# Kernel optimization log

Measured on AMD Instinct MI355X. Metric: run time of the kernel, lower is better.

Reference implementation:

```python
import jax, jax.numpy as jnp
import numpy as np

DIM = 256
NH = 8
HD = DIM // NH          # 32
KD = HD // 2            # 16, attn_ratio=0.5
SCALE = KD ** -0.5
EPS = 1e-3              # BatchNorm2d eps=0.001
B, H, W = 8, 32, 32


def _bn(x, g, b, m, v):
    # inference-mode BatchNorm2d over channel axis 1 of NCHW
    inv = g / jnp.sqrt(v + EPS)
    return x * inv[None, :, None, None] + (b - m * inv)[None, :, None, None]


def setup_inputs() -> dict:
    key = jax.random.key(0)
    ks = jax.random.split(key, 16)
    h_out = DIM + 2 * NH * KD  # 512
    return {
        "x": jax.random.normal(ks[0], (B, DIM, H, W), jnp.float32),
        "qkv_w": jax.random.normal(ks[1], (h_out, DIM), jnp.float32) * 0.05,
        "qkv_g": jax.random.uniform(ks[2], (h_out,), jnp.float32, 0.5, 1.5),
        "qkv_b": jax.random.normal(ks[3], (h_out,), jnp.float32) * 0.1,
        "qkv_m": jax.random.normal(ks[4], (h_out,), jnp.float32) * 0.1,
        "qkv_v": jax.random.uniform(ks[5], (h_out,), jnp.float32, 0.5, 1.5),
        "pe_w": jax.random.normal(ks[6], (DIM, 1, 3, 3), jnp.float32) * 0.1,
        "pe_g": jax.random.uniform(ks[7], (DIM,), jnp.float32, 0.5, 1.5),
        "pe_b": jax.random.normal(ks[8], (DIM,), jnp.float32) * 0.1,
        "pe_m": jax.random.normal(ks[9], (DIM,), jnp.float32) * 0.1,
        "pe_v": jax.random.uniform(ks[10], (DIM,), jnp.float32, 0.5, 1.5),
        "proj_w": jax.random.normal(ks[11], (DIM, DIM), jnp.float32) * 0.05,
        "proj_g": jax.random.uniform(ks[12], (DIM,), jnp.float32, 0.5, 1.5),
        "proj_b": jax.random.normal(ks[13], (DIM,), jnp.float32) * 0.1,
        "proj_m": jax.random.normal(ks[14], (DIM,), jnp.float32) * 0.1,
        "proj_v": jax.random.uniform(ks[15], (DIM,), jnp.float32, 0.5, 1.5),
    }


def reference(x, qkv_w, qkv_g, qkv_b, qkv_m, qkv_v,
              pe_w, pe_g, pe_b, pe_m, pe_v,
              proj_w, proj_g, proj_b, proj_m, proj_v):
    b, c, h, w = x.shape
    n = h * w
    # qkv: 1x1 conv (no bias) + BN, act=Identity
    qkv = _bn(jnp.einsum('oc,bchw->bohw', qkv_w, x), qkv_g, qkv_b, qkv_m, qkv_v)
    qkv = qkv.reshape(b, NH, 2 * KD + HD, n)
    q, k, v = jnp.split(qkv, [KD, 2 * KD], axis=2)  # [b,nh,kd,n],[b,nh,kd,n],[b,nh,hd,n]
    # attn = q^T @ k * scale, softmax over keys (last dim)
    attn = jax.nn.softmax(jnp.einsum('bhkn,bhkm->bhnm', q, k) * SCALE, axis=-1)
    # v @ attn^T -> [b,nh,hd,n]
    out = jnp.einsum('bhdj,bhij->bhdi', v, attn).reshape(b, c, h, w)
    # depthwise 3x3 positional branch on v (reshaped to spatial)
    v_sp = v.reshape(b, c, h, w)
    pe = jax.lax.conv_general_dilated(v_sp, pe_w, window_strides=(1, 1),
                                      padding=((1, 1), (1, 1)),
                                      feature_group_count=c)
    pe = _bn(pe, pe_g, pe_b, pe_m, pe_v)
    x_attn = out + pe
    # final 1x1 projection + BN
    return _bn(jnp.einsum('oc,bchw->bohw', proj_w, x_attn),
               proj_g, proj_b, proj_m, proj_v)
```

## Files before the change

kernel.cpp:

```cpp
#include <hip/hip_runtime.h>
#include <hip/hip_bf16.h>

#define B_    8
#define DIM_  256
#define NH_   8
#define HD_   32
#define KD_   16
#define HOUT_ 512
#define N_    1024
#define SCALE_ 0.25f
#define EPS_  1e-3f

typedef unsigned short u16;
typedef unsigned int   u32;
typedef __attribute__((ext_vector_type(8)))  short short8;
typedef __attribute__((ext_vector_type(4)))  float f32x4;
typedef __attribute__((ext_vector_type(16))) float f32x16;

union H4 { uint2 u; u16 e[4]; };
union FragU { uint4 u; short8 s; };

__device__ __forceinline__ float b2f(u16 u) {
    union { unsigned int i; float f; } c;
    c.i = ((unsigned int)u) << 16;
    return c.f;
}

__device__ __forceinline__ u16 f2b(float f) {
    union { float f; unsigned int i; } c;
    c.f = f;
    unsigned int x = c.i;
    return (u16)((x + 0x7fffu + ((x >> 16) & 1u)) >> 16);
}

__global__ __launch_bounds__(256) void k_pre(
    const float* __restrict__ x, u16* __restrict__ xT,
    const float* __restrict__ qw, const float* __restrict__ pw,
    const float* __restrict__ pew,
    const float* __restrict__ qg, const float* __restrict__ qb,
    const float* __restrict__ qm, const float* __restrict__ qv,
    const float* __restrict__ pg, const float* __restrict__ pb,
    const float* __restrict__ pm, const float* __restrict__ pv,
    const float* __restrict__ eg, const float* __restrict__ eb,
    const float* __restrict__ em, const float* __restrict__ ev,
    u16* __restrict__ wq_bf, u16* __restrict__ wp_bf,
    float2* __restrict__ bnq, float2* __restrict__ bnp,
    float* __restrict__ wpe, float* __restrict__ bnpe)
{
    __shared__ float t_s[64][65];
    int blk = blockIdx.x;
    int t = threadIdx.x;
    if (blk >= 512) {
        int i = (blk - 512) * 256 + t;
        wq_bf[i] = f2b(qw[i]);
        if (i < 65536) wp_bf[i] = f2b(pw[i]);
        if (i < 512) {
            float inv = qg[i] / sqrtf(qv[i] + EPS_);
            bnq[i] = make_float2(inv, qb[i] - qm[i] * inv);
        } else if (i < 768) {
            int o = i - 512;
            float inv = pg[o] / sqrtf(pv[o] + EPS_);
            bnp[o] = make_float2(inv, pb[o] - pm[o] * inv);
        }
        if (i < 2304) {
            int c = i / 9;
            float inv = eg[c] / sqrtf(ev[c] + EPS_);
            wpe[i] = pew[i] * inv;
            if (i % 9 == 0) bnpe[c] = eb[c] - em[c] * inv;
        }
        return;
    }
    int nt = blk & 15, ct = (blk >> 4) & 3, b = blk >> 6;
    int c0 = ct * 64, n0 = nt * 64;
    #pragma unroll
    for (int i = 0; i < 16; ++i) {
        int idx = i * 256 + t;
        int c = idx >> 6, n = idx & 63;
        t_s[n][c] = x[(size_t)(b * DIM_ + c0 + c) * N_ + n0 + n];
    }
    __syncthreads();
    #pragma unroll
    for (int i = 0; i < 16; ++i) {
        int idx = i * 256 + t;
        int n = idx >> 6, c = idx & 63;
        xT[(size_t)(b * N_ + n0 + n) * DIM_ + c0 + c] = f2b(t_s[n][c]);
    }
}

__global__ __launch_bounds__(256) void k_qkv(
    const u16* __restrict__ xT, const u16* __restrict__ wbf,
    const float2* __restrict__ bn, u16* __restrict__ qkv)
{
    int blk = blockIdx.x;
    int nb = blk & 7, ob = (blk >> 3) & 7, b = blk >> 6;
    int t = threadIdx.x;
    int wv_ = t >> 6, lane = t & 63, quad = lane >> 4, l16 = lane & 15;
    int o_base = ob * 64 + (wv_ & 1) * 32;
    int n_base = nb * 128 + (wv_ >> 1) * 64;

    f32x4 acc[2][4];
    #pragma unroll
    for (int ot = 0; ot < 2; ++ot)
        #pragma unroll
        for (int nt = 0; nt < 4; ++nt) acc[ot][nt] = (f32x4){0.f, 0.f, 0.f, 0.f};

    const u16* xb = xT + (size_t)b * N_ * DIM_;
    for (int c0 = 0; c0 < DIM_; c0 += 32) {
        short8 af[2];
        #pragma unroll
        for (int ot = 0; ot < 2; ++ot)
            af[ot] = *(const short8*)(wbf + (size_t)(o_base + ot * 16 + l16) * DIM_ + c0 + quad * 8);
        short8 bf[4];
        #pragma unroll
        for (int nt = 0; nt < 4; ++nt)
            bf[nt] = *(const short8*)(xb + (size_t)(n_base + nt * 16 + l16) * DIM_ + c0 + quad * 8);
        #pragma unroll
        for (int ot = 0; ot < 2; ++ot)
            #pragma unroll
            for (int nt = 0; nt < 4; ++nt)
                acc[ot][nt] = __builtin_amdgcn_mfma_f32_16x16x32_bf16(af[ot], bf[nt], acc[ot][nt], 0, 0, 0);
    }
    #pragma unroll
    for (int ot = 0; ot < 2; ++ot)
        #pragma unroll
        for (int r = 0; r < 4; ++r) {
            int o = o_base + ot * 16 + quad * 4 + r;
            float2 ib = bn[o];
            u16* dst = qkv + (size_t)(b * HOUT_ + o) * N_ + n_base + l16;
            #pragma unroll
            for (int nt = 0; nt < 4; ++nt)
                dst[nt * 16] = f2b(acc[ot][nt][r] * ib.x + ib.y);
        }
}

struct MainS { u16 q_t[64][24]; u16 k_t[2][256][24]; };
struct EpiS  { u16 o_acc[2][32][66]; float l_s[2][64]; float v_pe[128][33]; };
union  SmemU { MainS m; EpiS e; };

__global__ __launch_bounds__(256) void k_attn(
    const u16* __restrict__ qkv, const float* __restrict__ wpe,
    const float* __restrict__ bnpe, u16* __restrict__ xattnT)
{
    __shared__ SmemU su;
    int blk = blockIdx.x;
    int qb = blk & 15;
    int h  = (blk >> 4) & 7;
    int b  = blk >> 7;
    int t    = threadIdx.x;
    int wv_  = t >> 6;
    int lane = t & 63;
    int q5   = lane & 31;
    int hw   = lane >> 5;
    int kh   = wv_ >> 1;
    int qt   = wv_ & 1;
    const u16* base = qkv + (size_t)(b * HOUT_ + h * 64) * N_;
    int q0g = qb * 64;

    {
        int q = t & 63, d4 = (t >> 6) * 4;
        H4 hh;
        #pragma unroll
        for (int i = 0; i < 4; ++i)
            hh.e[i] = f2b(b2f(base[(size_t)(d4 + i) * N_ + q0g + q]) * SCALE_);
        *(uint2*)&su.m.q_t[q][d4] = hh.u;
    }
    __syncthreads();

    short8 qf = *(const short8*)&su.m.q_t[qt * 32 + q5][hw * 8];

    f32x16 oacc = {0.f,0.f,0.f,0.f, 0.f,0.f,0.f,0.f, 0.f,0.f,0.f,0.f, 0.f,0.f,0.f,0.f};
    float l_lane = 0.f;

    for (int ch = 0; ch < 2; ++ch) {
        __syncthreads();
        {
            #pragma unroll
            for (int s2 = 0; s2 < 2; ++s2) {
                int key = s2 * 512 + ch * 256 + t;
                #pragma unroll
                for (int d4 = 0; d4 < 16; d4 += 4) {
                    H4 hh;
                    #pragma unroll
                    for (int i = 0; i < 4; ++i)
                        hh.e[i] = base[(size_t)(16 + d4 + i) * N_ + key];
                    *(uint2*)&su.m.k_t[s2][t][d4] = hh.u;
                }
            }
        }
        __syncthreads();

        #pragma unroll 2
        for (int tile = 0; tile < 8; ++tile) {
            int key0 = kh * 512 + ch * 256 + tile * 32;
            short8 kf = *(const short8*)&su.m.k_t[kh][tile * 32 + q5][hw * 8];
            f32x16 z = {0.f,0.f,0.f,0.f, 0.f,0.f,0.f,0.f, 0.f,0.f,0.f,0.f, 0.f,0.f,0.f,0.f};
            f32x16 sT = __builtin_amdgcn_mfma_f32_32x32x16_bf16(kf, qf, z, 0, 0, 0);
            u32 pk[8];
            #pragma unroll
            for (int j = 0; j < 8; ++j) {
                float p0 = __expf(fminf(sT[2 * j], 80.f));
                float p1 = __expf(fminf(sT[2 * j + 1], 80.f));
                l_lane += p0 + p1;
                pk[j] = (u32)f2b(p0) | ((u32)f2b(p1) << 16);
            }
            #pragma unroll
            for (int s = 0; s < 2; ++s) {
                u32 s0 = hw ? pk[4 * s + 0] : pk[4 * s + 2];
                u32 s1 = hw ? pk[4 * s + 1] : pk[4 * s + 3];
                u32 r0 = __shfl_xor(s0, 32);
                u32 r1 = __shfl_xor(s1, 32);
                FragU pf;
                pf.u.x = hw ? r0 : pk[4 * s + 0];
                pf.u.y = hw ? r1 : pk[4 * s + 1];
                pf.u.z = hw ? pk[4 * s + 2] : r0;
                pf.u.w = hw ? pk[4 * s + 3] : r1;
                const u16* vsrc = base + (size_t)(32 + q5) * N_ + key0 + s * 16 + hw * 8;
                short8 vf = *(const short8*)vsrc;
                oacc = __builtin_amdgcn_mfma_f32_32x32x16_bf16(vf, pf.s, oacc, 0, 0, 0);
            }
        }
    }

    float l_q = l_lane + __shfl_xor(l_lane, 32);
    __syncthreads();

    {
        int qg = qt * 32 + q5;
        #pragma unroll
        for (int r = 0; r < 16; ++r) {
            int d = (r & 3) + 8 * (r >> 2) + 4 * hw;
            su.e.o_acc[kh][d][qg] = f2b(oacc[r]);
        }
        if (hw == 0) su.e.l_s[kh][qg] = l_q;
    }
    {
        int ybase = qb * 2 - 1;
        #pragma unroll
        for (int i = 0; i < 16; ++i) {
            int idx = i * 256 + t;
            int d = idx >> 7, px = idx & 127;
            int y = ybase + (px >> 5);
            float v = 0.f;
            if (y >= 0 && y < 32)
                v = b2f(base[(size_t)(32 + d) * N_ + y * 32 + (px & 31)]);
            su.e.v_pe[px][d] = v;
        }
    }
    __syncthreads();

    {
        int d = t & 31, pxg = t >> 5;
        int c = h * 32 + d;
        float w9[9];
        #pragma unroll
        for (int k = 0; k < 9; ++k) w9[k] = wpe[c * 9 + k];
        float beta = bnpe[c];
        #pragma unroll
        for (int ii = 0; ii < 8; ++ii) {
            int pl = pxg * 8 + ii;
            int xx0 = pl & 31;
            float s = beta;
            #pragma unroll
            for (int dy = -1; dy <= 1; ++dy) {
                #pragma unroll
                for (int dx = -1; dx <= 1; ++dx) {
                    int xx = xx0 + dx;
                    if (xx < 0 || xx > 31) continue;
                    s += w9[(dy + 1) * 3 + (dx + 1)] * su.e.v_pe[pl + 32 + dy * 32 + dx][d];
                }
            }
            float o = b2f(su.e.o_acc[0][d][pl]) + b2f(su.e.o_acc[1][d][pl]);
            float l = su.e.l_s[0][pl] + su.e.l_s[1][pl];
            xattnT[(size_t)(b * N_ + q0g + pl) * DIM_ + c] = f2b(o / fmaxf(l, 1e-30f) + s);
        }
    }
}

__global__ __launch_bounds__(256) void k_proj(
    const u16* __restrict__ xattnT, const u16* __restrict__ wbf,
    const float2* __restrict__ bn, float* __restrict__ out)
{
    int blk = blockIdx.x;
    int nb = blk & 15, ob = (blk >> 4) & 3, b = blk >> 6;
    int t = threadIdx.x;
    int wv_ = t >> 6, lane = t & 63, quad = lane >> 4, l16 = lane & 15;
    int o_base = ob * 64 + (wv_ & 1) * 32;
    int n_base = nb * 64 + (wv_ >> 1) * 32;

    f32x4 acc[2][2];
    #pragma unroll
    for (int ot = 0; ot < 2; ++ot)
        #pragma unroll
        for (int nt = 0; nt < 2; ++nt) acc[ot][nt] = (f32x4){0.f, 0.f, 0.f, 0.f};

    const u16* xb = xattnT + (size_t)b * N_ * DIM_;
    for (int c0 = 0; c0 < DIM_; c0 += 32) {
        short8 af[2];
        #pragma unroll
        for (int ot = 0; ot < 2; ++ot)
            af[ot] = *(const short8*)(wbf + (size_t)(o_base + ot * 16 + l16) * DIM_ + c0 + quad * 8);
        short8 bf[2];
        #pragma unroll
        for (int nt = 0; nt < 2; ++nt)
            bf[nt] = *(const short8*)(xb + (size_t)(n_base + nt * 16 + l16) * DIM_ + c0 + quad * 8);
        #pragma unroll
        for (int ot = 0; ot < 2; ++ot)
            #pragma unroll
            for (int nt = 0; nt < 2; ++nt)
                acc[ot][nt] = __builtin_amdgcn_mfma_f32_16x16x32_bf16(af[ot], bf[nt], acc[ot][nt], 0, 0, 0);
    }
    #pragma unroll
    for (int ot = 0; ot < 2; ++ot)
        #pragma unroll
        for (int r = 0; r < 4; ++r) {
            int o = o_base + ot * 16 + quad * 4 + r;
            float2 ib = bn[o];
            float* dst = out + (size_t)(b * DIM_ + o) * N_ + n_base + l16;
            #pragma unroll
            for (int nt = 0; nt < 2; ++nt)
                dst[nt * 16] = acc[ot][nt][r] * ib.x + ib.y;
        }
}

extern "C" void kernel_launch(void* const* d_in, const int* in_sizes, int n_in,
                              void* d_out, int out_size, void* d_ws, size_t ws_size,
                              hipStream_t stream)
{
    const float* x      = (const float*)d_in[0];
    const float* qkv_w  = (const float*)d_in[1];
    const float* qkv_g  = (const float*)d_in[2];
    const float* qkv_b  = (const float*)d_in[3];
    const float* qkv_m  = (const float*)d_in[4];
    const float* qkv_v  = (const float*)d_in[5];
    const float* pe_w   = (const float*)d_in[6];
    const float* pe_g   = (const float*)d_in[7];
    const float* pe_b   = (const float*)d_in[8];
    const float* pe_m   = (const float*)d_in[9];
    const float* pe_v   = (const float*)d_in[10];
    const float* proj_w = (const float*)d_in[11];
    const float* proj_g = (const float*)d_in[12];
    const float* proj_b = (const float*)d_in[13];
    const float* proj_m = (const float*)d_in[14];
    const float* proj_v = (const float*)d_in[15];
    float* out = (float*)d_out;

    char* p = (char*)d_ws;
    u16*    qkv    = (u16*)p;    p += (size_t)B_ * HOUT_ * N_ * sizeof(u16);
    u16*    xT     = (u16*)p;    p += (size_t)B_ * N_ * DIM_ * sizeof(u16);
    u16*    xattnT = (u16*)p;    p += (size_t)B_ * N_ * DIM_ * sizeof(u16);
    u16*    wq_bf  = (u16*)p;    p += (size_t)HOUT_ * DIM_ * sizeof(u16);
    u16*    wp_bf  = (u16*)p;    p += (size_t)DIM_ * DIM_ * sizeof(u16);
    float2* bnq    = (float2*)p; p += 512 * sizeof(float2);
    float2* bnp    = (float2*)p; p += 256 * sizeof(float2);
    float*  wpe    = (float*)p;  p += 2304 * sizeof(float);
    float*  bnpe   = (float*)p;

    hipLaunchKernelGGL(k_pre, dim3(1024), dim3(256), 0, stream,
                       x, xT, qkv_w, proj_w, pe_w,
                       qkv_g, qkv_b, qkv_m, qkv_v,
                       proj_g, proj_b, proj_m, proj_v,
                       pe_g, pe_b, pe_m, pe_v,
                       wq_bf, wp_bf, bnq, bnp, wpe, bnpe);
    hipLaunchKernelGGL(k_qkv, dim3(512), dim3(256), 0, stream,
                       xT, wq_bf, bnq, qkv);
    hipLaunchKernelGGL(k_attn, dim3(1024), dim3(256), 0, stream,
                       qkv, wpe, bnpe, xattnT);
    hipLaunchKernelGGL(k_proj, dim3(512), dim3(256), 0, stream,
                       xattnT, wp_bf, bnp, out);
}
```

Baseline: 152.1 us.

## Drop preprocessing kernel; convert fp32 inputs and fold BN params inside consumers

Removes the k_pre launch that transposed x to bf16 and pre-converted weights and BN constants. k_qkv now reads fp32 x directly with strided per-element loads and converts to bf16 on the fly. The q scale is folded into the BN affine for the first 16 output channels of each block, and k_attn and k_proj compute their BN and depthwise weights into shared memory themselves. This saves a launch and a full write and read of xT, but x is now loaded with strided scalar accesses and weights are reconverted redundantly in every block.

```diff
diff --git a/kernel.cpp b/kernel.cpp
--- a/kernel.cpp
+++ b/kernel.cpp
@@ -19,6 +19,7 @@
 
 union H4 { uint2 u; u16 e[4]; };
 union FragU { uint4 u; short8 s; };
+union F8 { short8 s; u16 e[8]; };
 
 __device__ __forceinline__ float b2f(u16 u) {
     union { unsigned int i; float f; } c;
@@ -33,64 +34,29 @@
     return (u16)((x + 0x7fffu + ((x >> 16) & 1u)) >> 16);
 }
 
-__global__ __launch_bounds__(256) void k_pre(
-    const float* __restrict__ x, u16* __restrict__ xT,
-    const float* __restrict__ qw, const float* __restrict__ pw,
-    const float* __restrict__ pew,
+__device__ __forceinline__ short8 cvt8(const float* p) {
+    float4 a = ((const float4*)p)[0];
+    float4 b = ((const float4*)p)[1];
+    F8 f;
+    f.e[0] = f2b(a.x); f.e[1] = f2b(a.y); f.e[2] = f2b(a.z); f.e[3] = f2b(a.w);
+    f.e[4] = f2b(b.x); f.e[5] = f2b(b.y); f.e[6] = f2b(b.z); f.e[7] = f2b(b.w);
+    return f.s;
+}
+
+__device__ __forceinline__ short8 cvt8s(const float* p) {
+    F8 f;
+    #pragma unroll
+    for (int j = 0; j < 8; ++j) f.e[j] = f2b(p[(size_t)j * N_]);
+    return f.s;
+}
+
+__global__ __launch_bounds__(256) void k_qkv(
+    const float* __restrict__ x, const float* __restrict__ qw,
     const float* __restrict__ qg, const float* __restrict__ qb,
     const float* __restrict__ qm, const float* __restrict__ qv,
-    const float* __restrict__ pg, const float* __restrict__ pb,
-    const float* __restrict__ pm, const float* __restrict__ pv,
-    const float* __restrict__ eg, const float* __restrict__ eb,
-    const float* __restrict__ em, const float* __restrict__ ev,
-    u16* __restrict__ wq_bf, u16* __restrict__ wp_bf,
-    float2* __restrict__ bnq, float2* __restrict__ bnp,
-    float* __restrict__ wpe, float* __restrict__ bnpe)
+    u16* __restrict__ qkv)
 {
-    __shared__ float t_s[64][65];
-    int blk = blockIdx.x;
-    int t = threadIdx.x;
-    if (blk >= 512) {
-        int i = (blk - 512) * 256 + t;
-        wq_bf[i] = f2b(qw[i]);
-        if (i < 65536) wp_bf[i] = f2b(pw[i]);
-        if (i < 512) {
-            float inv = qg[i] / sqrtf(qv[i] + EPS_);
-            bnq[i] = make_float2(inv, qb[i] - qm[i] * inv);
-        } else if (i < 768) {
-            int o = i - 512;
-            float inv = pg[o] / sqrtf(pv[o] + EPS_);
-            bnp[o] = make_float2(inv, pb[o] - pm[o] * inv);
-        }
-        if (i < 2304) {
-            int c = i / 9;
-            float inv = eg[c] / sqrtf(ev[c] + EPS_);
-            wpe[i] = pew[i] * inv;
-            if (i % 9 == 0) bnpe[c] = eb[c] - em[c] * inv;
-        }
-        return;
-    }
-    int nt = blk & 15, ct = (blk >> 4) & 3, b = blk >> 6;
-    int c0 = ct * 64, n0 = nt * 64;
-    #pragma unroll
-    for (int i = 0; i < 16; ++i) {
-        int idx = i * 256 + t;
-        int c = idx >> 6, n = idx & 63;
-        t_s[n][c] = x[(size_t)(b * DIM_ + c0 + c) * N_ + n0 + n];
-    }
-    __syncthreads();
-    #pragma unroll
-    for (int i = 0; i < 16; ++i) {
-        int idx = i * 256 + t;
-        int n = idx >> 6, c = idx & 63;
-        xT[(size_t)(b * N_ + n0 + n) * DIM_ + c0 + c] = f2b(t_s[n][c]);
-    }
-}
-
-__global__ __launch_bounds__(256) void k_qkv(
-    const u16* __restrict__ xT, const u16* __restrict__ wbf,
-    const float2* __restrict__ bn, u16* __restrict__ qkv)
-{
+    __shared__ float2 bn_s[64];
     int blk = blockIdx.x;
     int nb = blk & 7, ob = (blk >> 3) & 7, b = blk >> 6;
     int t = threadIdx.x;
@@ -98,22 +64,31 @@
     int o_base = ob * 64 + (wv_ & 1) * 32;
     int n_base = nb * 128 + (wv_ >> 1) * 64;
 
+    if (t < 64) {
+        int o = ob * 64 + t;
+        float inv  = qg[o] / sqrtf(qv[o] + EPS_);
+        float beta = qb[o] - qm[o] * inv;
+        if (t < 16) { inv *= SCALE_; beta *= SCALE_; }
+        bn_s[t] = make_float2(inv, beta);
+    }
+    __syncthreads();
+
     f32x4 acc[2][4];
     #pragma unroll
     for (int ot = 0; ot < 2; ++ot)
         #pragma unroll
         for (int nt = 0; nt < 4; ++nt) acc[ot][nt] = (f32x4){0.f, 0.f, 0.f, 0.f};
 
-    const u16* xb = xT + (size_t)b * N_ * DIM_;
+    const float* xb = x + (size_t)b * DIM_ * N_;
     for (int c0 = 0; c0 < DIM_; c0 += 32) {
         short8 af[2];
         #pragma unroll
         for (int ot = 0; ot < 2; ++ot)
-            af[ot] = *(const short8*)(wbf + (size_t)(o_base + ot * 16 + l16) * DIM_ + c0 + quad * 8);
+            af[ot] = cvt8(qw + (size_t)(o_base + ot * 16 + l16) * DIM_ + c0 + quad * 8);
         short8 bf[4];
         #pragma unroll
         for (int nt = 0; nt < 4; ++nt)
-            bf[nt] = *(const short8*)(xb + (size_t)(n_base + nt * 16 + l16) * DIM_ + c0 + quad * 8);
+            bf[nt] = cvt8s(xb + (size_t)(c0 + quad * 8) * N_ + n_base + nt * 16 + l16);
         #pragma unroll
         for (int ot = 0; ot < 2; ++ot)
             #pragma unroll
@@ -124,9 +99,9 @@
     for (int ot = 0; ot < 2; ++ot)
         #pragma unroll
         for (int r = 0; r < 4; ++r) {
-            int o = o_base + ot * 16 + quad * 4 + r;
-            float2 ib = bn[o];
-            u16* dst = qkv + (size_t)(b * HOUT_ + o) * N_ + n_base + l16;
+            int ol = (wv_ & 1) * 32 + ot * 16 + quad * 4 + r;
+            float2 ib = bn_s[ol];
+            u16* dst = qkv + (size_t)(b * HOUT_ + ob * 64 + ol) * N_ + n_base + l16;
             #pragma unroll
             for (int nt = 0; nt < 4; ++nt)
                 dst[nt * 16] = f2b(acc[ot][nt][r] * ib.x + ib.y);
@@ -138,10 +113,13 @@
 union  SmemU { MainS m; EpiS e; };
 
 __global__ __launch_bounds__(256) void k_attn(
-    const u16* __restrict__ qkv, const float* __restrict__ wpe,
-    const float* __restrict__ bnpe, u16* __restrict__ xattnT)
+    const u16* __restrict__ qkv, const float* __restrict__ pew,
+    const float* __restrict__ eg, const float* __restrict__ eb,
+    const float* __restrict__ em, const float* __restrict__ ev,
+    u16* __restrict__ xattnT)
 {
     __shared__ SmemU su;
+    __shared__ float wpe_s[32][10];
     int blk = blockIdx.x;
     int qb = blk & 15;
     int h  = (blk >> 4) & 7;
@@ -156,12 +134,19 @@
     const u16* base = qkv + (size_t)(b * HOUT_ + h * 64) * N_;
     int q0g = qb * 64;
 
+    if (t < 32) {
+        int c = h * 32 + t;
+        float inv = eg[c] / sqrtf(ev[c] + EPS_);
+        #pragma unroll
+        for (int k = 0; k < 9; ++k) wpe_s[t][k] = pew[c * 9 + k] * inv;
+        wpe_s[t][9] = eb[c] - em[c] * inv;
+    }
     {
         int q = t & 63, d4 = (t >> 6) * 4;
         H4 hh;
         #pragma unroll
         for (int i = 0; i < 4; ++i)
-            hh.e[i] = f2b(b2f(base[(size_t)(d4 + i) * N_ + q0g + q]) * SCALE_);
+            hh.e[i] = base[(size_t)(d4 + i) * N_ + q0g + q];
         *(uint2*)&su.m.q_t[q][d4] = hh.u;
     }
     __syncthreads();
@@ -253,8 +238,8 @@
         int c = h * 32 + d;
         float w9[9];
         #pragma unroll
-        for (int k = 0; k < 9; ++k) w9[k] = wpe[c * 9 + k];
-        float beta = bnpe[c];
+        for (int k = 0; k < 9; ++k) w9[k] = wpe_s[d][k];
+        float beta = wpe_s[d][9];
         #pragma unroll
         for (int ii = 0; ii < 8; ++ii) {
             int pl = pxg * 8 + ii;
@@ -277,9 +262,12 @@
 }
 
 __global__ __launch_bounds__(256) void k_proj(
-    const u16* __restrict__ xattnT, const u16* __restrict__ wbf,
-    const float2* __restrict__ bn, float* __restrict__ out)
+    const u16* __restrict__ xattnT, const float* __restrict__ pw,
+    const float* __restrict__ pg, const float* __restrict__ pb,
+    const float* __restrict__ pm, const float* __restrict__ pv,
+    float* __restrict__ out)
 {
+    __shared__ float2 bn_s[64];
     int blk = blockIdx.x;
     int nb = blk & 15, ob = (blk >> 4) & 3, b = blk >> 6;
     int t = threadIdx.x;
@@ -287,6 +275,13 @@
     int o_base = ob * 64 + (wv_ & 1) * 32;
     int n_base = nb * 64 + (wv_ >> 1) * 32;
 
+    if (t < 64) {
+        int o = ob * 64 + t;
+        float inv = pg[o] / sqrtf(pv[o] + EPS_);
+        bn_s[t] = make_float2(inv, pb[o] - pm[o] * inv);
+    }
+    __syncthreads();
+
     f32x4 acc[2][2];
     #pragma unroll
     for (int ot = 0; ot < 2; ++ot)
@@ -298,7 +293,7 @@
         short8 af[2];
         #pragma unroll
         for (int ot = 0; ot < 2; ++ot)
-            af[ot] = *(const short8*)(wbf + (size_t)(o_base + ot * 16 + l16) * DIM_ + c0 + quad * 8);
+            af[ot] = cvt8(pw + (size_t)(o_base + ot * 16 + l16) * DIM_ + c0 + quad * 8);
         short8 bf[2];
         #pragma unroll
         for (int nt = 0; nt < 2; ++nt)
@@ -313,9 +308,9 @@
     for (int ot = 0; ot < 2; ++ot)
         #pragma unroll
         for (int r = 0; r < 4; ++r) {
-            int o = o_base + ot * 16 + quad * 4 + r;
-            float2 ib = bn[o];
-            float* dst = out + (size_t)(b * DIM_ + o) * N_ + n_base + l16;
+            int ol = (wv_ & 1) * 32 + ot * 16 + quad * 4 + r;
+            float2 ib = bn_s[ol];
+            float* dst = out + (size_t)(b * DIM_ + ob * 64 + ol) * N_ + n_base + l16;
             #pragma unroll
             for (int nt = 0; nt < 2; ++nt)
                 dst[nt * 16] = acc[ot][nt][r] * ib.x + ib.y;
@@ -345,26 +340,13 @@
     float* out = (float*)d_out;
 
     char* p = (char*)d_ws;
-    u16*    qkv    = (u16*)p;    p += (size_t)B_ * HOUT_ * N_ * sizeof(u16);
-    u16*    xT     = (u16*)p;    p += (size_t)B_ * N_ * DIM_ * sizeof(u16);
-    u16*    xattnT = (u16*)p;    p += (size_t)B_ * N_ * DIM_ * sizeof(u16);
-    u16*    wq_bf  = (u16*)p;    p += (size_t)HOUT_ * DIM_ * sizeof(u16);
-    u16*    wp_bf  = (u16*)p;    p += (size_t)DIM_ * DIM_ * sizeof(u16);
-    float2* bnq    = (float2*)p; p += 512 * sizeof(float2);
-    float2* bnp    = (float2*)p; p += 256 * sizeof(float2);
-    float*  wpe    = (float*)p;  p += 2304 * sizeof(float);
-    float*  bnpe   = (float*)p;
-
-    hipLaunchKernelGGL(k_pre, dim3(1024), dim3(256), 0, stream,
-                       x, xT, qkv_w, proj_w, pe_w,
-                       qkv_g, qkv_b, qkv_m, qkv_v,
-                       proj_g, proj_b, proj_m, proj_v,
-                       pe_g, pe_b, pe_m, pe_v,
-                       wq_bf, wp_bf, bnq, bnp, wpe, bnpe);
+    u16* qkv    = (u16*)p;  p += (size_t)B_ * HOUT_ * N_ * sizeof(u16);
+    u16* xattnT = (u16*)p;
+
     hipLaunchKernelGGL(k_qkv, dim3(512), dim3(256), 0, stream,
-                       xT, wq_bf, bnq, qkv);
+                       x, qkv_w, qkv_g, qkv_b, qkv_m, qkv_v, qkv);
     hipLaunchKernelGGL(k_attn, dim3(1024), dim3(256), 0, stream,
-                       qkv, wpe, bnpe, xattnT);
+                       qkv, pe_w, pe_g, pe_b, pe_m, pe_v, xattnT);
     hipLaunchKernelGGL(k_proj, dim3(512), dim3(256), 0, stream,
-                       xattnT, wp_bf, bnp, out);
-}
+                       xattnT, proj_w, proj_g, proj_b, proj_m, proj_v, out);
+}
```

Result: no change. 153.3 us (+0.7%).
